# Kernel tuning notes

Hardware: AMD Instinct MI355X
Metric: run time of the kernel (lower is better)

The kernel has to match this reference:

```python
import jax, jax.numpy as jnp
import numpy as np

B, S, H = 8, 2048, 1024   # batch, seq, hidden_size
E = 4                     # num_experts (world_size=1 -> all local)
C = 1024                  # kv_cache_size (cache_decrement=0 -> uniform pyramid)
R = 4                     # LoRA rank
ALPHA = 1.0
TOP_K = 2
TEMP = 1.0
KEEP = C // 2             # pyramid compressor keeps top-half by importance


def _lora(z, A, Bm):
    # LoRALayer: (z @ A) @ B scaled by alpha/rank
    return (z @ A) @ Bm * (ALPHA / A.shape[-1])


def setup_inputs() -> dict:
    key = jax.random.key(0)
    ks = jax.random.split(key, 24)
    w = lambda k, shp: jax.random.normal(k, shp, jnp.float32) * 0.02
    return {
        'x': jax.random.normal(ks[0], (B, S, H), jnp.float32),
        'query': jax.random.normal(ks[1], (B, S, H), jnp.float32),
        'Wg': w(ks[2], (H, E)), 'bg': jnp.zeros((E,), jnp.float32),
        'Wq': w(ks[3], (H, H)), 'bq': jnp.zeros((H,), jnp.float32),
        'Wk': w(ks[4], (H, H)), 'bk': jnp.zeros((H,), jnp.float32),
        'Aq': w(ks[5], (H, R)), 'Bq': w(ks[6], (R, H)),
        'Ak': w(ks[7], (H, R)), 'Bk': w(ks[8], (R, H)),
        'We': w(ks[9], (E, H, H)), 'be': jnp.zeros((E, H), jnp.float32),
        'Ae': w(ks[10], (E, H, R)), 'Be': w(ks[11], (E, R, H)),
        'Av': w(ks[12], (E, H, R)), 'Bv': w(ks[13], (E, R, H)),
        'cache_keys': jax.random.normal(ks[14], (E, C, H), jnp.float32),
        'cache_values': jax.random.normal(ks[15], (E, C, H), jnp.float32),
        'cache_imp': jax.random.uniform(ks[16], (E, C), jnp.float32),
    }


def reference(x, query, Wg, bg, Wq, bq, Wk, bk, Aq, Bq, Ak, Bk,
              We, be, Ae, Be, Av, Bv, cache_keys, cache_values, cache_imp):
    # ---- AdaptiveRouter: softmax gate, top-2 renormalized, load-balance loss ----
    probs = jax.nn.softmax((x @ Wg + bg) / TEMP, axis=-1)             # [B,S,E]
    tw, ti = jax.lax.top_k(probs, TOP_K)                              # [B,S,K]
    twn = tw / tw.sum(-1, keepdims=True)
    onehot = jax.nn.one_hot(ti, E, dtype=x.dtype)                     # [B,S,K,E]
    routing = jnp.einsum('bsk,bske->bse', twn, onehot)                # [B,S,E]
    lb_loss = E * jnp.sum(probs.mean((0, 1)) * onehot.mean((0, 1, 2)))

    # ---- compute_token_importance (query provided): LoRA-augmented q/k attention ----
    q = query @ Wq + bq + _lora(query, Aq, Bq)
    k = x @ Wk + bk + _lora(x, Ak, Bk)
    att = jax.nn.softmax(jnp.einsum('bqh,bkh->bqk', q, k) / np.sqrt(H).astype(np.float32), axis=-1)
    importance = att.sum(axis=1)                                      # [B,S] column sums

    # ---- per-expert LoRA forward + pyramid-compressed cache read ----
    def expert_fn(We_i, be_i, Ae_i, Be_i, Av_i, Bv_i, cv_i, ci_i):
        eo = x @ We_i + be_i + _lora(x, Ae_i, Be_i)                   # [B,S,H]
        idx = jax.lax.top_k(ci_i, KEEP)[1]                            # keep top-half by importance
        vals = cv_i[idx]                                              # [KEEP,H] irregular gather
        vals = vals + _lora(vals, Av_i, Bv_i)                         # value LoRA on compressed cache
        return eo + jax.lax.stop_gradient(vals.mean(0))               # cached values are detached

    outs = jax.vmap(expert_fn)(We, be, Ae, Be, Av, Bv, cache_values, cache_imp)  # [E,B,S,H]
    expert_output = jnp.einsum('ebsh,bse->bsh', outs, routing)

    # ---- cache update at ptr=0 (detached buffer mutation -> returned new state) ----
    sg = jax.lax.stop_gradient
    new_keys = cache_keys.at[:, 0].set(jnp.broadcast_to(sg(x.mean((0, 1))), (E, H)))
    new_values = cache_values.at[:, 0].set(sg(outs.mean((1, 2))))
    new_imp = cache_imp.at[:, 0].set(sg(importance.mean()))
    return expert_output, lb_loss, new_keys, new_values, new_imp
```

## Files before the change

kernel.cpp:

```cpp
#include <hip/hip_runtime.h>

constexpr int kH    = 1024;
constexpr int kNT   = 16384;
constexpr int kE    = 4;
constexpr int kC    = 1024;
constexpr int kR    = 4;
constexpr int kKeep = 512;
constexpr float kLoraScale = 0.25f;
constexpr int kCapTiles = 136;
constexpr int kCapRows  = kCapTiles * 128;
constexpr int kNB      = kNT / 256;

constexpr size_t WS_RW     = 0;
constexpr size_t WS_G      = 65536;
constexpr size_t WS_XSUM   = 393216;
constexpr size_t WS_SHADOW = 394240;
constexpr size_t WS_TU     = 394752;
constexpr size_t WS_VBAR   = 394784;
constexpr size_t WS_FX     = 398880;
constexpr size_t WS_NEWV0  = 402976;
constexpr size_t WS_MSK    = 407072;
constexpr size_t WS_GBASE  = 411168;
constexpr size_t WS_BHIST  = 411176;
constexpr size_t WS_BOFF   = 411560;
constexpr size_t WS_RTPID  = 411944;
constexpr size_t WS_TPID   = 412088;
constexpr size_t WS_GRO    = 428472;
constexpr size_t WS_PERM   = 444856;
constexpr size_t WS_WCAT   = 462264;
constexpr size_t WS_AEXT   = 482744;
constexpr size_t WS_AEXTG  = 744888;
constexpr size_t WS_BEXT   = 1023416;
constexpr size_t WS_WET    = 1039800;
constexpr size_t WS_XG     = 3136952;

constexpr size_t OUT_LB = 16777216;
constexpr size_t OUT_NK = 16777217;

typedef __attribute__((ext_vector_type(8))) short bf16x8;
typedef __attribute__((ext_vector_type(4))) float f32x4;

__device__ __forceinline__ float wred(float v) {
#pragma unroll
  for (int off = 32; off; off >>= 1) v += __shfl_xor(v, off);
  return v;
}

__device__ __forceinline__ ushort f2bf(float f) {
  unsigned int u = __float_as_uint(f);
  u += 0x7FFFu + ((u >> 16) & 1u);
  return (ushort)(u >> 16);
}

__device__ __forceinline__ void gload16(const ushort* g, ushort* l) {
  __builtin_amdgcn_global_load_lds(
      (const __attribute__((address_space(1))) unsigned int*)g,
      (__attribute__((address_space(3))) unsigned int*)l, 16, 0, 0);
}

__device__ __forceinline__ int pid_a(int pid) { return pid < 3 ? 0 : (pid < 5 ? 1 : 2); }
__device__ __forceinline__ int pid_b(int pid) { return pid < 3 ? pid + 1 : (pid < 5 ? pid - 1 : 3); }

__global__ __launch_bounds__(256) void prep_k(
    const float* __restrict__ Wg, const float* __restrict__ Ae,
    const float* __restrict__ ci, const float* __restrict__ x,
    float* __restrict__ wcat, float* __restrict__ msk,
    float* __restrict__ xsum, int* __restrict__ perm) {
  __shared__ float imp[kC];
  const int b = blockIdx.x, tid = threadIdx.x;
  if (b < 80) {
    const int idx = b * 256 + tid;
    const int c = idx >> 10, k = idx & 1023;
    float v;
    if (c < 4) v = Wg[(size_t)k * 4 + c];
    else {
      const int e = (c - 4) >> 2, r = (c - 4) & 3;
      v = Ae[((size_t)e * kH + k) * kR + r];
    }
    wcat[(size_t)c * kH + k] = v;
  } else if (b < 96) {
    const int e = (b - 80) >> 2, part = (b - 80) & 3;
    const int c = part * 256 + tid;
    for (int i = tid; i < kC; i += 256) imp[i] = ci[(size_t)e * kC + i];
    __syncthreads();
    const float v = imp[c];
    int rank = 0;
    for (int c2 = 0; c2 < kC; ++c2) {
      const float v2 = imp[c2];
      rank += (v2 > v) || (v2 == v && c2 < c);
    }
    msk[(size_t)e * kC + c] = (rank < kKeep) ? 1.0f : 0.0f;
  } else if (b < 352) {
    const int rg = b - 96;
    const float* xp = x + (size_t)rg * 64 * kH + tid * 4;
    float s0 = 0.f, s1 = 0.f, s2 = 0.f, s3 = 0.f;
    for (int r = 0; r < 64; ++r) {
      const float4 v = *(const float4*)(xp + (size_t)r * kH);
      s0 += v.x; s1 += v.y; s2 += v.z; s3 += v.w;
    }
    atomicAdd(&xsum[tid * 4 + 0], s0);
    atomicAdd(&xsum[tid * 4 + 1], s1);
    atomicAdd(&xsum[tid * 4 + 2], s2);
    atomicAdd(&xsum[tid * 4 + 3], s3);
  } else {
    const int i = (b - 352) * 256 + tid;
    perm[i] = -1;
  }
}

__global__ __launch_bounds__(256) void router_gemm_k(
    const float* __restrict__ x, const float* __restrict__ wcat,
    float* __restrict__ G) {
  __shared__ float xs_l[128][64];
  __shared__ float wt_l[20][64];
  const int tid = threadIdx.x;
  const int t0 = blockIdx.x * 128;
  const int tok = tid & 127, half = tid >> 7, cb = half * 10;
  float acc[10] = {};
  for (int kc = 0; kc < 16; ++kc) {
#pragma unroll
    for (int i = 0; i < 8; ++i) {
      const int idx = tid + i * 256;
      const int stok = idx >> 4, sslot = idx & 15;
      const float4 v =
          *(const float4*)(x + (size_t)(t0 + stok) * kH + kc * 64 + sslot * 4);
      *(float4*)&xs_l[stok][((sslot + stok) & 15) * 4] = v;
    }
    for (int idx = tid; idx < 320; idx += 256) {
      const int c = idx >> 4, slot = idx & 15;
      *(float4*)&wt_l[c][slot * 4] =
          *(const float4*)(wcat + (size_t)c * kH + kc * 64 + slot * 4);
    }
    __syncthreads();
#pragma unroll
    for (int k4 = 0; k4 < 16; ++k4) {
      const float4 xv = *(const float4*)&xs_l[tok][((k4 + tok) & 15) * 4];
#pragma unroll
      for (int j = 0; j < 10; ++j) {
        const float4 wv = *(const float4*)&wt_l[cb + j][k4 * 4];
        acc[j] += xv.x * wv.x + xv.y * wv.y + xv.z * wv.z + xv.w * wv.w;
      }
    }
    __syncthreads();
  }
#pragma unroll
  for (int j = 0; j < 10; ++j)
    G[(size_t)(cb + j) * kNT + t0 + tok] = acc[j];
}

__global__ __launch_bounds__(256) void router_fin_k(
    const float* __restrict__ G, const float* __restrict__ bg,
    float* __restrict__ rw, float* __restrict__ shadow,
    int* __restrict__ tpid, int* __restrict__ bhist,
    ushort* __restrict__ aext) {
  __shared__ float swacc[8];
  __shared__ int ihist[6];
  const int tid = threadIdx.x;
  const int t = blockIdx.x * 256 + tid;
  const int lane = tid & 63;
  if (tid < 8) swacc[tid] = 0.f;
  if (tid < 6) ihist[tid] = 0;
  __syncthreads();
  float lg[kE];
#pragma unroll
  for (int e = 0; e < kE; ++e) lg[e] = G[(size_t)e * kNT + t] + bg[e];
  float la[kE][kR];
#pragma unroll
  for (int e = 0; e < kE; ++e)
#pragma unroll
    for (int r = 0; r < kR; ++r)
      la[e][r] = G[(size_t)(4 + e * 4 + r) * kNT + t];
  const float mx = fmaxf(fmaxf(lg[0], lg[1]), fmaxf(lg[2], lg[3]));
  float ex[kE], se = 0.f;
#pragma unroll
  for (int e = 0; e < kE; ++e) { ex[e] = __expf(lg[e] - mx); se += ex[e]; }
  float pr[kE];
#pragma unroll
  for (int e = 0; e < kE; ++e) pr[e] = ex[e] / se;
  int e1 = 0;
#pragma unroll
  for (int e = 1; e < kE; ++e) if (pr[e] > pr[e1]) e1 = e;
  int e2 = (e1 == 0) ? 1 : 0;
#pragma unroll
  for (int e = 0; e < kE; ++e) if (e != e1 && pr[e] > pr[e2]) e2 = e;
  const float s2 = pr[e1] + pr[e2];
  float rwv[kE] = {0.f, 0.f, 0.f, 0.f};
  rwv[e1] = pr[e1] / s2; rwv[e2] = pr[e2] / s2;
  *(float4*)(rw + (size_t)t * kE) = make_float4(rwv[0], rwv[1], rwv[2], rwv[3]);
  const int lo = min(e1, e2), hi = max(e1, e2);
  const int pid = (lo == 0) ? hi - 1 : ((lo == 1) ? hi + 1 : 5);
  tpid[t] = pid;
  __align__(16) ushort o[32];
#pragma unroll
  for (int e = 0; e < kE; ++e) o[e] = f2bf(rwv[e]);
#pragma unroll
  for (int e = 0; e < kE; ++e)
#pragma unroll
    for (int r = 0; r < kR; ++r)
      o[4 + e * 4 + r] = f2bf(kLoraScale * rwv[e] * la[e][r]);
#pragma unroll
  for (int i = 20; i < 32; ++i) o[i] = 0;
#pragma unroll
  for (int q = 0; q < 4; ++q)
    *(float4*)&aext[(size_t)t * 32 + q * 8] = *(float4*)&o[q * 8];
  float vals[8];
#pragma unroll
  for (int e = 0; e < kE; ++e) {
    vals[e] = pr[e];
    vals[4 + e] = ((e == e1) ? 1.f : 0.f) + ((e == e2) ? 1.f : 0.f);
  }
#pragma unroll
  for (int j = 0; j < 8; ++j) {
    vals[j] = wred(vals[j]);
    if (lane == 0) atomicAdd(&swacc[j], vals[j]);
  }
  atomicAdd(&ihist[pid], 1);
  __syncthreads();
  if (tid < 8) atomicAdd(&shadow[(blockIdx.x & 63) * 8 + tid], swacc[tid]);
  if (tid < 6) bhist[blockIdx.x * 6 + tid] = ihist[tid];
}

__global__ __launch_bounds__(256) void pscan_k(const int* __restrict__ bhist,
                                               int* __restrict__ gbase,
                                               int* __restrict__ boff,
                                               int* __restrict__ rtpid) {
  __shared__ int pcnt_s[6];
  const int tid = threadIdx.x;
  if (tid < 6) {
    int run = 0;
    for (int b = 0; b < kNB; ++b) {
      boff[b * 6 + tid] = run;
      run += bhist[b * 6 + tid];
    }
    pcnt_s[tid] = run;
  }
  __syncthreads();
  if (tid == 0) {
    int base = 0;
    for (int g = 0; g < 6; ++g) {
      gbase[g] = base;
      const int tiles = (pcnt_s[g] + 127) >> 7;
      for (int ti = 0; ti < tiles; ++ti) rtpid[(base >> 7) + ti] = g;
      base += tiles << 7;
    }
    for (int i = base >> 7; i < kCapTiles; ++i) rtpid[i] = -1;
  }
  __syncthreads();
  if (tid < 6) {
    const int gb = gbase[tid];
    for (int b = 0; b < kNB; ++b) boff[b * 6 + tid] += gb;
  }
}

__global__ __launch_bounds__(256) void slot_k(const int* __restrict__ tpid,
                                              const int* __restrict__ boff,
                                              int* __restrict__ gro,
                                              int* __restrict__ perm) {
  __shared__ int wcnt[4][6];
  const int tid = threadIdx.x, w = tid >> 6, lane = tid & 63;
  const int t = blockIdx.x * 256 + tid;
  const int pid = tpid[t];
  unsigned long long mymask = 0;
  int cnt[6];
#pragma unroll
  for (int g = 0; g < 6; ++g) {
    const unsigned long long m = __ballot(pid == g);
    cnt[g] = __popcll(m);
    if (g == pid) mymask = m;
  }
  if (lane < 6) wcnt[w][lane] = cnt[lane];
  const int rank_in_wave =
      __popcll(mymask & ((lane == 63) ? 0x7FFFFFFFFFFFFFFFULL
                                      : ((1ULL << lane) - 1ULL)));
  __syncthreads();
  int base = 0;
  for (int w2 = 0; w2 < w; ++w2) base += wcnt[w2][pid];
  const int grow = boff[blockIdx.x * 6 + pid] + base + rank_in_wave;
  gro[t] = grow;
  perm[grow] = t;
}

__global__ __launch_bounds__(256) void aux3_k(
    const float* __restrict__ x, const float* __restrict__ rw,
    const int* __restrict__ tpid, const ushort* __restrict__ aext,
    const int* __restrict__ gro, ushort* __restrict__ xg,
    ushort* __restrict__ aextg, const float* __restrict__ We,
    const float* __restrict__ xsum, ushort* __restrict__ wet,
    float* __restrict__ fx, const float* __restrict__ cv,
    const float* __restrict__ msk, float* __restrict__ vbar) {
  __shared__ ushort tile[64][72];
  __shared__ float fxl[16][64];
  __shared__ float xml[64];
  const int b = blockIdx.x, tid = threadIdx.x;
  if (b < 4096) {
    const int wave = tid >> 6, lane = tid & 63;
    const int t = b * 4 + wave;
    const int pid = tpid[t];
    const int grow = gro[t];
    const float wa = rw[(size_t)t * 4 + pid_a(pid)];
    const float wb = rw[(size_t)t * 4 + pid_b(pid)];
#pragma unroll
    for (int q = 0; q < 4; ++q) {
      const int c = q * 256 + lane * 4;
      const float4 v = *(const float4*)(x + (size_t)t * kH + c);
      ushort4 ua, ub;
      ua.x = f2bf(wa * v.x); ua.y = f2bf(wa * v.y);
      ua.z = f2bf(wa * v.z); ua.w = f2bf(wa * v.w);
      ub.x = f2bf(wb * v.x); ub.y = f2bf(wb * v.y);
      ub.z = f2bf(wb * v.z); ub.w = f2bf(wb * v.w);
      *(ushort4*)(xg + (size_t)grow * 2048 + c) = ua;
      *(ushort4*)(xg + (size_t)grow * 2048 + 1024 + c) = ub;
    }
    if (lane < 4)
      *(float4*)&aextg[(size_t)grow * 32 + lane * 8] =
          *(const float4*)&aext[(size_t)t * 32 + lane * 8];
  } else if (b < 5120) {
    const int bp = b - 4096;
    const int jb = bp & 15, kb = (bp >> 4) & 15, e = bp >> 8;
    const int rr = tid >> 4, cq = tid & 15;
    if (tid < 64) xml[tid] = xsum[kb * 64 + tid] * (1.0f / kNT);
    __syncthreads();
    float fxp[4] = {};
#pragma unroll
    for (int p = 0; p < 4; ++p) {
      const int k = kb * 64 + p * 16 + rr;
      const float4 v = *(const float4*)&We[((size_t)e * kH + k) * kH + jb * 64 + cq * 4];
      tile[p * 16 + rr][cq * 4 + 0] = f2bf(v.x);
      tile[p * 16 + rr][cq * 4 + 1] = f2bf(v.y);
      tile[p * 16 + rr][cq * 4 + 2] = f2bf(v.z);
      tile[p * 16 + rr][cq * 4 + 3] = f2bf(v.w);
      const float xm = xml[p * 16 + rr];
      fxp[0] += xm * v.x; fxp[1] += xm * v.y; fxp[2] += xm * v.z; fxp[3] += xm * v.w;
    }
    *(float4*)&fxl[rr][cq * 4] = make_float4(fxp[0], fxp[1], fxp[2], fxp[3]);
    __syncthreads();
    if (tid < 64) {
      float s = 0.f;
#pragma unroll
      for (int r2 = 0; r2 < 16; ++r2) s += fxl[r2][tid];
      atomicAdd(&fx[(size_t)e * kH + jb * 64 + tid], s);
    }
#pragma unroll
    for (int p = 0; p < 4; ++p) {
      const int j = jb * 64 + p * 16 + rr;
      ushort4 u;
      u.x = tile[cq * 4 + 0][p * 16 + rr];
      u.y = tile[cq * 4 + 1][p * 16 + rr];
      u.z = tile[cq * 4 + 2][p * 16 + rr];
      u.w = tile[cq * 4 + 3][p * 16 + rr];
      *(ushort4*)&wet[((size_t)e * kH + j) * kH + kb * 64 + cq * 4] = u;
    }
  } else {
    const int bp = b - 5120;
    const int e = bp & 3, rc = bp >> 2;
    const float* base = cv + (size_t)e * kC * kH + (size_t)rc * 32 * kH + tid * 4;
    const float* m = msk + (size_t)e * kC + rc * 32;
    float s0 = 0.f, s1 = 0.f, s2 = 0.f, s3 = 0.f;
#pragma unroll 8
    for (int r = 0; r < 32; ++r) {
      const float mr = m[r];
      const float4 v = *(const float4*)(base + (size_t)r * kH);
      s0 += mr * v.x; s1 += mr * v.y; s2 += mr * v.z; s3 += mr * v.w;
    }
    const float sc = 1.0f / kKeep;
    atomicAdd(&vbar[(size_t)e * kH + tid * 4 + 0], s0 * sc);
    atomicAdd(&vbar[(size_t)e * kH + tid * 4 + 1], s1 * sc);
    atomicAdd(&vbar[(size_t)e * kH + tid * 4 + 2], s2 * sc);
    atomicAdd(&vbar[(size_t)e * kH + tid * 4 + 3], s3 * sc);
  }
}

__global__ __launch_bounds__(256) void tufin_k(
    const float* __restrict__ vbar, const float* __restrict__ xsum,
    const float* __restrict__ Av, const float* __restrict__ Ae,
    const float* __restrict__ be, const float* __restrict__ Bv,
    const float* __restrict__ Bee, const float* __restrict__ fx,
    float* __restrict__ newv0_ws, ushort* __restrict__ bext) {
  __shared__ float red[256];
  __shared__ float tus[8];
  const int e = blockIdx.x, tid = threadIdx.x;
  float p[8] = {};
#pragma unroll
  for (int q = 0; q < 4; ++q) {
    const int h = tid * 4 + q;
    const float vb = vbar[(size_t)e * kH + h];
    const float xm = xsum[h] * (1.0f / kNT);
    const float4 av = *(const float4*)(Av + ((size_t)e * kH + h) * kR);
    const float4 ae = *(const float4*)(Ae + ((size_t)e * kH + h) * kR);
    p[0] += vb * av.x; p[1] += vb * av.y; p[2] += vb * av.z; p[3] += vb * av.w;
    p[4] += xm * ae.x; p[5] += xm * ae.y; p[6] += xm * ae.z; p[7] += xm * ae.w;
  }
#pragma unroll
  for (int j = 0; j < 8; ++j) {
    red[tid] = p[j]; __syncthreads();
    for (int s2 = 128; s2; s2 >>= 1) {
      if (tid < s2) red[tid] += red[tid + s2];
      __syncthreads();
    }
    if (tid == 0) tus[j] = red[0];
    __syncthreads();
  }
  float t_[4], u_[4];
#pragma unroll
  for (int r = 0; r < kR; ++r) { t_[r] = tus[r]; u_[r] = tus[4 + r]; }
#pragma unroll
  for (int q = 0; q < 4; ++q) {
    const int col = q * 256 + tid;
    float lv = 0.f, le = 0.f;
#pragma unroll
    for (int r = 0; r < kR; ++r) {
      lv += t_[r] * Bv[((size_t)e * kR + r) * kH + col];
      le += u_[r] * Bee[((size_t)e * kR + r) * kH + col];
    }
    const float mv = vbar[(size_t)e * kH + col] + kLoraScale * lv;
    const float bias = be[(size_t)e * kH + col] + mv;
    newv0_ws[(size_t)e * kH + col] = fx[(size_t)e * kH + col] + kLoraScale * le + bias;
    bext[(size_t)col * 32 + e] = f2bf(bias);
#pragma unroll
    for (int r = 0; r < kR; ++r)
      bext[(size_t)col * 32 + 4 + e * 4 + r] =
          f2bf(Bee[((size_t)e * kR + r) * kH + col]);
    if (e == 0)
#pragma unroll
      for (int i = 20; i < 32; ++i) bext[(size_t)col * 32 + i] = 0;
  }
}

__global__ __launch_bounds__(256, 2) void gemm_copyfix_k(
    const ushort* __restrict__ xg, const ushort* __restrict__ wet,
    const ushort* __restrict__ aextg, const ushort* __restrict__ bext,
    const int* __restrict__ rtpid, const int* __restrict__ perm,
    const float* __restrict__ ck, const float* __restrict__ cv,
    const float* __restrict__ ci, const float* __restrict__ xsum,
    const float* __restrict__ newv0, const float* __restrict__ shadow,
    float* __restrict__ out) {
  __shared__ __align__(16) ushort As[2][128 * 32];
  __shared__ __align__(16) ushort Bs[2][128 * 32];
  __shared__ int perm_s[128];
  const int tid = threadIdx.x;
  if (blockIdx.x >= 1088) {
    const size_t NK = (size_t)kE * kC * kH;
    const size_t idx = (size_t)(blockIdx.x - 1088) * 256 + tid;
    if (idx < NK) {
      const size_t c = (idx >> 10) & (kC - 1), h = idx & (kH - 1);
      out[OUT_NK + idx] = (c == 0) ? xsum[h] * (1.0f / kNT) : ck[idx];
    } else if (idx < 2 * NK) {
      const size_t j = idx - NK;
      const size_t e = j >> 20, c = (j >> 10) & (kC - 1), h = j & (kH - 1);
      out[OUT_NK + idx] = (c == 0) ? newv0[e * kH + h] : cv[j];
    } else if (idx < 2 * NK + (size_t)kE * kC) {
      const size_t j = idx - 2 * NK;
      out[OUT_NK + idx] = ((j & (kC - 1)) == 0) ? 1.0f : ci[j];
    } else if (idx == 2 * NK + (size_t)kE * kC) {
      float lb = 0.f;
#pragma unroll
      for (int e = 0; e < kE; ++e) {
        float ps = 0.f, cn = 0.f;
        for (int s2 = 0; s2 < 64; ++s2) {
          ps += shadow[s2 * 8 + e];
          cn += shadow[s2 * 8 + 4 + e];
        }
        lb += (ps * (1.0f / kNT)) * (cn * (1.0f / (kNT * 2.0f)));
      }
      out[OUT_LB] = kE * lb;
    }
    return;
  }
  const int bid = blockIdx.x;
  const int gid = (bid & 7) * 136 + (bid >> 3);
  const int rt = gid >> 3, ct = gid & 7;
  const int pid = rtpid[rt];
  if (pid < 0) return;
  const int lane = tid & 63, wave = tid >> 6;
  const int wm = wave >> 1, wn = wave & 1;
  const int r0 = rt * 128, c0 = ct * 128;
  const int ea = pid_a(pid), eb = pid_b(pid);
  if (tid < 128) perm_s[tid] = perm[r0 + tid];

  const int srow = lane >> 2;
  const int sslot = lane & 3;

  auto stage = [&](int buf, int kt) {
#pragma unroll
    for (int i = 0; i < 2; ++i) {
      const int j0 = wave * 32 + i * 16;
      const int r = j0 + srow;
      const int slot = sslot ^ ((r >> 1) & 3);
      const ushort* srcA;
      const ushort* srcB;
      if (kt < 64) {
        const int e = (kt < 32) ? ea : eb;
        const int ko = ((kt & 31) * 32) + ((kt < 32) ? 0 : 1024);
        srcA = xg + (size_t)(r0 + r) * 2048 + ko + slot * 8;
        srcB = wet + ((size_t)e * kH + c0 + r) * kH + (kt & 31) * 32 + slot * 8;
      } else {
        srcA = aextg + (size_t)(r0 + r) * 32 + slot * 8;
        srcB = bext + (size_t)(c0 + r) * 32 + slot * 8;
      }
      gload16(srcA, &As[buf][j0 * 32]);
      gload16(srcB, &Bs[buf][j0 * 32]);
    }
  };

  f32x4 acc[4][4] = {};
  stage(0, 0);
  asm volatile("s_waitcnt vmcnt(0)" ::: "memory");
  __syncthreads();

  const int rA = lane & 15;
  const int fslot = lane >> 4;
  int buf = 0;
  for (int kt = 0; kt <= 64; ++kt) {
    if (kt < 64) stage(buf ^ 1, kt + 1);
    bf16x8 a[4], b[4];
#pragma unroll
    for (int m = 0; m < 4; ++m) {
      const int r = wm * 64 + m * 16 + rA;
      const int sl = fslot ^ ((r >> 1) & 3);
      a[m] = *(const bf16x8*)&As[buf][r * 32 + sl * 8];
    }
#pragma unroll
    for (int n = 0; n < 4; ++n) {
      const int r = wn * 64 + n * 16 + rA;
      const int sl = fslot ^ ((r >> 1) & 3);
      b[n] = *(const bf16x8*)&Bs[buf][r * 32 + sl * 8];
    }
#pragma unroll
    for (int m = 0; m < 4; ++m)
#pragma unroll
      for (int n = 0; n < 4; ++n)
        acc[m][n] = __builtin_amdgcn_mfma_f32_16x16x32_bf16(a[m], b[n], acc[m][n], 0, 0, 0);
    if (kt < 64) asm volatile("s_waitcnt vmcnt(0)" ::: "memory");
    __syncthreads();
    buf ^= 1;
  }

#pragma unroll
  for (int m = 0; m < 4; ++m) {
#pragma unroll
    for (int v = 0; v < 4; ++v) {
      const int rl = wm * 64 + m * 16 + (lane >> 4) * 4 + v;
      const int tok = perm_s[rl];
      if (tok >= 0) {
        float* orow = out + (size_t)tok * kH + c0 + wn * 64 + (lane & 15);
#pragma unroll
        for (int n = 0; n < 4; ++n) orow[n * 16] = acc[m][n][v];
      }
    }
  }
}

extern "C" void kernel_launch(void* const* d_in, const int* in_sizes, int n_in,
                              void* d_out, int out_size, void* d_ws, size_t ws_size,
                              hipStream_t stream) {
  const float* x   = (const float*)d_in[0];
  const float* Wg  = (const float*)d_in[2];
  const float* bg  = (const float*)d_in[3];
  const float* We  = (const float*)d_in[12];
  const float* be  = (const float*)d_in[13];
  const float* Ae  = (const float*)d_in[14];
  const float* Bee = (const float*)d_in[15];
  const float* Av  = (const float*)d_in[16];
  const float* Bv  = (const float*)d_in[17];
  const float* ck  = (const float*)d_in[18];
  const float* cv  = (const float*)d_in[19];
  const float* ci  = (const float*)d_in[20];
  float* ws  = (float*)d_ws;
  float* out = (float*)d_out;

  int* tpid  = (int*)(ws + WS_TPID);
  int* bhist = (int*)(ws + WS_BHIST);
  int* boff  = (int*)(ws + WS_BOFF);
  int* gbase = (int*)(ws + WS_GBASE);
  int* rtpid = (int*)(ws + WS_RTPID);
  int* gro   = (int*)(ws + WS_GRO);
  int* perm  = (int*)(ws + WS_PERM);
  ushort* aext  = (ushort*)(ws + WS_AEXT);
  ushort* aextg = (ushort*)(ws + WS_AEXTG);
  ushort* bext  = (ushort*)(ws + WS_BEXT);
  ushort* wet   = (ushort*)(ws + WS_WET);
  ushort* xg    = (ushort*)(ws + WS_XG);

  hipMemsetAsync(ws + WS_XSUM, 0, 9760 * sizeof(float), stream);
  prep_k<<<420, 256, 0, stream>>>(Wg, Ae, ci, x, ws + WS_WCAT, ws + WS_MSK,
                                  ws + WS_XSUM, perm);
  router_gemm_k<<<kNT / 128, 256, 0, stream>>>(x, ws + WS_WCAT, ws + WS_G);
  router_fin_k<<<kNB, 256, 0, stream>>>(ws + WS_G, bg, ws + WS_RW,
                                        ws + WS_SHADOW, tpid, bhist, aext);
  pscan_k<<<1, 256, 0, stream>>>(bhist, gbase, boff, rtpid);
  slot_k<<<kNB, 256, 0, stream>>>(tpid, boff, gro, perm);
  aux3_k<<<5248, 256, 0, stream>>>(x, ws + WS_RW, tpid, aext, gro, xg, aextg,
                                   We, ws + WS_XSUM, wet, ws + WS_FX, cv,
                                   ws + WS_MSK, ws + WS_VBAR);
  tufin_k<<<kE, 256, 0, stream>>>(ws + WS_VBAR, ws + WS_XSUM, Av, Ae, be, Bv,
                                  Bee, ws + WS_FX, ws + WS_NEWV0, bext);
  gemm_copyfix_k<<<1088 + 32785, 256, 0, stream>>>(
      xg, wet, aextg, bext, rtpid, perm, ck, cv, ci, ws + WS_XSUM,
      ws + WS_NEWV0, ws + WS_SHADOW, out);
}
```

Before: 321.3 us.

## Fuse router GEMM with finalize and fold prefix scan into slot kernel

The router logits GEMM now finishes the softmax/top-2/aext work in the same kernel via shared memory, removing the global G buffer round trip and one launch. The single-block prefix-scan kernel is removed: each slot block recomputes its own per-group offsets and totals from the 128 per-block histograms, and block 0 writes the tile-to-group map. This cuts two launches and a serial scan, at the cost of redundant histogram reads per block and only half the threads being active in the finalize phase.

```diff
diff --git a/kernel.cpp b/kernel.cpp
--- a/kernel.cpp
+++ b/kernel.cpp
@@ -9,10 +9,9 @@
 constexpr float kLoraScale = 0.25f;
 constexpr int kCapTiles = 136;
 constexpr int kCapRows  = kCapTiles * 128;
-constexpr int kNB      = kNT / 256;
+constexpr int kNRB     = kNT / 128;
 
 constexpr size_t WS_RW     = 0;
-constexpr size_t WS_G      = 65536;
 constexpr size_t WS_XSUM   = 393216;
 constexpr size_t WS_SHADOW = 394240;
 constexpr size_t WS_TU     = 394752;
@@ -22,7 +21,6 @@
 constexpr size_t WS_MSK    = 407072;
 constexpr size_t WS_GBASE  = 411168;
 constexpr size_t WS_BHIST  = 411176;
-constexpr size_t WS_BOFF   = 411560;
 constexpr size_t WS_RTPID  = 411944;
 constexpr size_t WS_TPID   = 412088;
 constexpr size_t WS_GRO    = 428472;
@@ -108,14 +106,25 @@
   }
 }
 
-__global__ __launch_bounds__(256) void router_gemm_k(
+__global__ __launch_bounds__(256) void rgf_k(
     const float* __restrict__ x, const float* __restrict__ wcat,
-    float* __restrict__ G) {
-  __shared__ float xs_l[128][64];
+    const float* __restrict__ bg, float* __restrict__ rw,
+    float* __restrict__ shadow, int* __restrict__ tpid,
+    int* __restrict__ bhist, ushort* __restrict__ aext) {
+  union Smem {
+    float xs[128][64];
+    float gsh[128][20];
+  };
+  __shared__ Smem sm;
   __shared__ float wt_l[20][64];
+  __shared__ float swacc[8];
+  __shared__ int ihist[6];
   const int tid = threadIdx.x;
   const int t0 = blockIdx.x * 128;
   const int tok = tid & 127, half = tid >> 7, cb = half * 10;
+  const int lane = tid & 63;
+  if (tid < 8) swacc[tid] = 0.f;
+  if (tid < 6) ihist[tid] = 0;
   float acc[10] = {};
   for (int kc = 0; kc < 16; ++kc) {
 #pragma unroll
@@ -124,7 +133,7 @@
       const int stok = idx >> 4, sslot = idx & 15;
       const float4 v =
           *(const float4*)(x + (size_t)(t0 + stok) * kH + kc * 64 + sslot * 4);
-      *(float4*)&xs_l[stok][((sslot + stok) & 15) * 4] = v;
+      *(float4*)&sm.xs[stok][((sslot + stok) & 15) * 4] = v;
     }
     for (int idx = tid; idx < 320; idx += 256) {
       const int c = idx >> 4, slot = idx & 15;
@@ -134,7 +143,7 @@
     __syncthreads();
 #pragma unroll
     for (int k4 = 0; k4 < 16; ++k4) {
-      const float4 xv = *(const float4*)&xs_l[tok][((k4 + tok) & 15) * 4];
+      const float4 xv = *(const float4*)&sm.xs[tok][((k4 + tok) & 15) * 4];
 #pragma unroll
       for (int j = 0; j < 10; ++j) {
         const float4 wv = *(const float4*)&wt_l[cb + j][k4 * 4];
@@ -144,121 +153,87 @@
     __syncthreads();
   }
 #pragma unroll
-  for (int j = 0; j < 10; ++j)
-    G[(size_t)(cb + j) * kNT + t0 + tok] = acc[j];
-}
-
-__global__ __launch_bounds__(256) void router_fin_k(
-    const float* __restrict__ G, const float* __restrict__ bg,
-    float* __restrict__ rw, float* __restrict__ shadow,
-    int* __restrict__ tpid, int* __restrict__ bhist,
-    ushort* __restrict__ aext) {
-  __shared__ float swacc[8];
-  __shared__ int ihist[6];
-  const int tid = threadIdx.x;
-  const int t = blockIdx.x * 256 + tid;
-  const int lane = tid & 63;
-  if (tid < 8) swacc[tid] = 0.f;
-  if (tid < 6) ihist[tid] = 0;
+  for (int j = 0; j < 10; ++j) sm.gsh[tok][cb + j] = acc[j];
   __syncthreads();
-  float lg[kE];
-#pragma unroll
-  for (int e = 0; e < kE; ++e) lg[e] = G[(size_t)e * kNT + t] + bg[e];
-  float la[kE][kR];
-#pragma unroll
-  for (int e = 0; e < kE; ++e)
-#pragma unroll
-    for (int r = 0; r < kR; ++r)
-      la[e][r] = G[(size_t)(4 + e * 4 + r) * kNT + t];
-  const float mx = fmaxf(fmaxf(lg[0], lg[1]), fmaxf(lg[2], lg[3]));
-  float ex[kE], se = 0.f;
-#pragma unroll
-  for (int e = 0; e < kE; ++e) { ex[e] = __expf(lg[e] - mx); se += ex[e]; }
-  float pr[kE];
-#pragma unroll
-  for (int e = 0; e < kE; ++e) pr[e] = ex[e] / se;
-  int e1 = 0;
-#pragma unroll
-  for (int e = 1; e < kE; ++e) if (pr[e] > pr[e1]) e1 = e;
-  int e2 = (e1 == 0) ? 1 : 0;
-#pragma unroll
-  for (int e = 0; e < kE; ++e) if (e != e1 && pr[e] > pr[e2]) e2 = e;
-  const float s2 = pr[e1] + pr[e2];
-  float rwv[kE] = {0.f, 0.f, 0.f, 0.f};
-  rwv[e1] = pr[e1] / s2; rwv[e2] = pr[e2] / s2;
-  *(float4*)(rw + (size_t)t * kE) = make_float4(rwv[0], rwv[1], rwv[2], rwv[3]);
-  const int lo = min(e1, e2), hi = max(e1, e2);
-  const int pid = (lo == 0) ? hi - 1 : ((lo == 1) ? hi + 1 : 5);
-  tpid[t] = pid;
-  __align__(16) ushort o[32];
-#pragma unroll
-  for (int e = 0; e < kE; ++e) o[e] = f2bf(rwv[e]);
-#pragma unroll
-  for (int e = 0; e < kE; ++e)
-#pragma unroll
-    for (int r = 0; r < kR; ++r)
-      o[4 + e * 4 + r] = f2bf(kLoraScale * rwv[e] * la[e][r]);
-#pragma unroll
-  for (int i = 20; i < 32; ++i) o[i] = 0;
-#pragma unroll
-  for (int q = 0; q < 4; ++q)
-    *(float4*)&aext[(size_t)t * 32 + q * 8] = *(float4*)&o[q * 8];
-  float vals[8];
-#pragma unroll
-  for (int e = 0; e < kE; ++e) {
-    vals[e] = pr[e];
-    vals[4 + e] = ((e == e1) ? 1.f : 0.f) + ((e == e2) ? 1.f : 0.f);
-  }
-#pragma unroll
-  for (int j = 0; j < 8; ++j) {
-    vals[j] = wred(vals[j]);
-    if (lane == 0) atomicAdd(&swacc[j], vals[j]);
-  }
-  atomicAdd(&ihist[pid], 1);
+  if (tid < 128) {
+    const int t = t0 + tid;
+    float lg[kE];
+#pragma unroll
+    for (int e = 0; e < kE; ++e) lg[e] = sm.gsh[tid][e] + bg[e];
+    float la[kE][kR];
+#pragma unroll
+    for (int e = 0; e < kE; ++e)
+#pragma unroll
+      for (int r = 0; r < kR; ++r) la[e][r] = sm.gsh[tid][4 + e * 4 + r];
+    const float mx = fmaxf(fmaxf(lg[0], lg[1]), fmaxf(lg[2], lg[3]));
+    float ex[kE], se = 0.f;
+#pragma unroll
+    for (int e = 0; e < kE; ++e) { ex[e] = __expf(lg[e] - mx); se += ex[e]; }
+    float pr[kE];
+#pragma unroll
+    for (int e = 0; e < kE; ++e) pr[e] = ex[e] / se;
+    int e1 = 0;
+#pragma unroll
+    for (int e = 1; e < kE; ++e) if (pr[e] > pr[e1]) e1 = e;
+    int e2 = (e1 == 0) ? 1 : 0;
+#pragma unroll
+    for (int e = 0; e < kE; ++e) if (e != e1 && pr[e] > pr[e2]) e2 = e;
+    const float s2 = pr[e1] + pr[e2];
+    float rwv[kE] = {0.f, 0.f, 0.f, 0.f};
+    rwv[e1] = pr[e1] / s2; rwv[e2] = pr[e2] / s2;
+    *(float4*)(rw + (size_t)t * kE) = make_float4(rwv[0], rwv[1], rwv[2], rwv[3]);
+    const int lo = min(e1, e2), hi = max(e1, e2);
+    const int pid = (lo == 0) ? hi - 1 : ((lo == 1) ? hi + 1 : 5);
+    tpid[t] = pid;
+    __align__(16) ushort o[32];
+#pragma unroll
+    for (int e = 0; e < kE; ++e) o[e] = f2bf(rwv[e]);
+#pragma unroll
+    for (int e = 0; e < kE; ++e)
+#pragma unroll
+      for (int r = 0; r < kR; ++r)
+        o[4 + e * 4 + r] = f2bf(kLoraScale * rwv[e] * la[e][r]);
+#pragma unroll
+    for (int i = 20; i < 32; ++i) o[i] = 0;
+#pragma unroll
+    for (int q = 0; q < 4; ++q)
+      *(float4*)&aext[(size_t)t * 32 + q * 8] = *(float4*)&o[q * 8];
+    float vals[8];
+#pragma unroll
+    for (int e = 0; e < kE; ++e) {
+      vals[e] = pr[e];
+      vals[4 + e] = ((e == e1) ? 1.f : 0.f) + ((e == e2) ? 1.f : 0.f);
+    }
+#pragma unroll
+    for (int j = 0; j < 8; ++j) {
+      vals[j] = wred(vals[j]);
+      if (lane == 0) atomicAdd(&swacc[j], vals[j]);
+    }
+    atomicAdd(&ihist[pid], 1);
+  }
   __syncthreads();
   if (tid < 8) atomicAdd(&shadow[(blockIdx.x & 63) * 8 + tid], swacc[tid]);
   if (tid < 6) bhist[blockIdx.x * 6 + tid] = ihist[tid];
 }
 
-__global__ __launch_bounds__(256) void pscan_k(const int* __restrict__ bhist,
-                                               int* __restrict__ gbase,
-                                               int* __restrict__ boff,
-                                               int* __restrict__ rtpid) {
-  __shared__ int pcnt_s[6];
-  const int tid = threadIdx.x;
+__global__ __launch_bounds__(128) void slot_k(const int* __restrict__ tpid,
+                                              const int* __restrict__ bhist,
+                                              int* __restrict__ gro,
+                                              int* __restrict__ perm,
+                                              int* __restrict__ rtpid) {
+  __shared__ int wcnt[2][6];
+  __shared__ int offs[6], totals[6];
+  const int tid = threadIdx.x, w = tid >> 6, lane = tid & 63;
   if (tid < 6) {
-    int run = 0;
-    for (int b = 0; b < kNB; ++b) {
-      boff[b * 6 + tid] = run;
-      run += bhist[b * 6 + tid];
-    }
-    pcnt_s[tid] = run;
-  }
-  __syncthreads();
-  if (tid == 0) {
-    int base = 0;
-    for (int g = 0; g < 6; ++g) {
-      gbase[g] = base;
-      const int tiles = (pcnt_s[g] + 127) >> 7;
-      for (int ti = 0; ti < tiles; ++ti) rtpid[(base >> 7) + ti] = g;
-      base += tiles << 7;
-    }
-    for (int i = base >> 7; i < kCapTiles; ++i) rtpid[i] = -1;
-  }
-  __syncthreads();
-  if (tid < 6) {
-    const int gb = gbase[tid];
-    for (int b = 0; b < kNB; ++b) boff[b * 6 + tid] += gb;
-  }
-}
-
-__global__ __launch_bounds__(256) void slot_k(const int* __restrict__ tpid,
-                                              const int* __restrict__ boff,
-                                              int* __restrict__ gro,
-                                              int* __restrict__ perm) {
-  __shared__ int wcnt[4][6];
-  const int tid = threadIdx.x, w = tid >> 6, lane = tid & 63;
-  const int t = blockIdx.x * 256 + tid;
+    int off = 0, tot = 0;
+    for (int b2 = 0; b2 < kNRB; ++b2) {
+      const int v = bhist[b2 * 6 + tid];
+      if (b2 < (int)blockIdx.x) off += v;
+      tot += v;
+    }
+    offs[tid] = off; totals[tid] = tot;
+  }
+  const int t = blockIdx.x * 128 + tid;
   const int pid = tpid[t];
   unsigned long long mymask = 0;
   int cnt[6];
@@ -273,11 +248,21 @@
       __popcll(mymask & ((lane == 63) ? 0x7FFFFFFFFFFFFFFFULL
                                       : ((1ULL << lane) - 1ULL)));
   __syncthreads();
-  int base = 0;
-  for (int w2 = 0; w2 < w; ++w2) base += wcnt[w2][pid];
-  const int grow = boff[blockIdx.x * 6 + pid] + base + rank_in_wave;
+  const int base = (w == 1) ? wcnt[0][pid] : 0;
+  int gbase = 0;
+  for (int g = 0; g < pid; ++g) gbase += ((totals[g] + 127) >> 7) << 7;
+  const int grow = gbase + offs[pid] + base + rank_in_wave;
   gro[t] = grow;
   perm[grow] = t;
+  if (blockIdx.x == 0 && tid == 0) {
+    int bb = 0;
+    for (int g = 0; g < 6; ++g) {
+      const int tiles = (totals[g] + 127) >> 7;
+      for (int ti = 0; ti < tiles; ++ti) rtpid[(bb >> 7) + ti] = g;
+      bb += tiles << 7;
+    }
+    for (int i = bb >> 7; i < kCapTiles; ++i) rtpid[i] = -1;
+  }
 }
 
 __global__ __launch_bounds__(256) void aux3_k(
@@ -570,8 +555,6 @@
 
   int* tpid  = (int*)(ws + WS_TPID);
   int* bhist = (int*)(ws + WS_BHIST);
-  int* boff  = (int*)(ws + WS_BOFF);
-  int* gbase = (int*)(ws + WS_GBASE);
   int* rtpid = (int*)(ws + WS_RTPID);
   int* gro   = (int*)(ws + WS_GRO);
   int* perm  = (int*)(ws + WS_PERM);
@@ -584,11 +567,9 @@
   hipMemsetAsync(ws + WS_XSUM, 0, 9760 * sizeof(float), stream);
   prep_k<<<420, 256, 0, stream>>>(Wg, Ae, ci, x, ws + WS_WCAT, ws + WS_MSK,
                                   ws + WS_XSUM, perm);
-  router_gemm_k<<<kNT / 128, 256, 0, stream>>>(x, ws + WS_WCAT, ws + WS_G);
-  router_fin_k<<<kNB, 256, 0, stream>>>(ws + WS_G, bg, ws + WS_RW,
-                                        ws + WS_SHADOW, tpid, bhist, aext);
-  pscan_k<<<1, 256, 0, stream>>>(bhist, gbase, boff, rtpid);
-  slot_k<<<kNB, 256, 0, stream>>>(tpid, boff, gro, perm);
+  rgf_k<<<kNRB, 256, 0, stream>>>(x, ws + WS_WCAT, bg, ws + WS_RW,
+                                  ws + WS_SHADOW, tpid, bhist, aext);
+  slot_k<<<kNRB, 128, 0, stream>>>(tpid, bhist, gro, perm, rtpid);
   aux3_k<<<5248, 256, 0, stream>>>(x, ws + WS_RW, tpid, aext, gro, xg, aextg,
                                    We, ws + WS_XSUM, wet, ws + WS_FX, cv,
                                    ws + WS_MSK, ws + WS_VBAR);
```

New measurement: 325.2 us. No clear change (+1.2%).
